# Kernel tuning notes

Hardware: AMD Instinct MI355X
Metric: run time of the kernel (lower is better)

The kernel has to match this reference:

```python
import jax, jax.numpy as jnp
import numpy as np

T, B, H, W_IMG = 8, 4, 128, 128
NUM_CLS = 21
LEAK = 0.99   # config.leak_mem
THR = 1.0     # config.def_threshold
EPS = 1e-4    # BatchNorm2d eps


@jax.custom_vjp
def spike(mem):
    # Heaviside spike with 'Linear' surrogate gradient
    return (mem > THR).astype(mem.dtype)

def _spike_fwd(mem):
    return spike(mem), mem

def _spike_bwd(mem, g):
    # triangular (linear) surrogate around threshold
    return (g * jnp.maximum(0.0, 1.0 - jnp.abs(mem - THR)),)

spike.defvjp(_spike_fwd, _spike_bwd)


def conv(x, w, pad, dil=1):
    return jax.lax.conv_general_dilated(
        x, w, window_strides=(1, 1), padding=[(pad, pad), (pad, pad)],
        rhs_dilation=(dil, dil), dimension_numbers=('NCHW', 'OIHW', 'NCHW'))


def bn_apply(x, bn_t):
    # bn_t: [3, C] = (gamma, running_mean, running_var); bias=None in the model
    g, mu, var = bn_t[0], bn_t[1], bn_t[2]
    inv = (g / jnp.sqrt(var + EPS))[None, :, None, None]
    return (x - mu[None, :, None, None]) * inv


def avgpool(x):
    # AvgPool2d(kernel=3, stride=2, padding=1), count_include_pad=True -> /9
    s = jax.lax.reduce_window(x, 0.0, jax.lax.add, (1, 1, 3, 3), (1, 1, 2, 2),
                              [(0, 0), (0, 0), (1, 1), (1, 1)])
    return s / 9.0


def lif(x, w, bn_t, mem, pad, dil=1):
    # mem = leak*mem + BN_t(conv(x)); spike; soft reset by threshold
    out = bn_apply(conv(x, w, pad, dil), bn_t)
    mem = LEAK * mem + out
    s = spike(mem)
    return mem - THR * s, s


def _forward(x, u, W0, W1, W2, W3, W4, W5, W6, W7, W8,
             bn0, bn1, bn2, bn3, bn4, bn5, bn6, bn7):
    # Poisson generator: spike when u <= |x|, carrying sign of x. [T,B,3,H,W]
    spk_in = jnp.where(u <= jnp.abs(x)[None], jnp.sign(x)[None], 0.0)
    z = lambda c, h: jnp.zeros((B, c, h, h), x.dtype)
    init = (z(64, 128), z(64, 128), z(128, 64), z(128, 64),
            z(256, 32), z(256, 32), z(256, 32), z(1024, 32), z(NUM_CLS, 32))

    def step(carry, xs):
        m0, m1, m2, m3, m4, m5, m6, m7, macc = carry
        sp, b0, b1, b2, b3, b4, b5, b6, b7 = xs
        m0, o = lif(sp, W0, b0, m0, 1)
        m1, o = lif(o, W1, b1, m1, 1)
        o = avgpool(o)                      # 128 -> 64
        m2, o = lif(o, W2, b2, m2, 1)
        m3, o = lif(o, W3, b3, m3, 1)
        o = avgpool(o)                      # 64 -> 32
        m4, o = lif(o, W4, b4, m4, 1)
        m5, o = lif(o, W5, b5, m5, 2, 2)    # atrous256
        m6, o = lif(o, W6, b6, m6, 2, 2)    # atrous256
        m7, o = lif(o, W7, b7, m7, 12, 12)  # classifier atrous1024
        macc = macc + conv(o, W8, 0)        # output layer accumulates voltage
        return (m0, m1, m2, m3, m4, m5, m6, m7, macc), None

    carry, _ = jax.lax.scan(step, init, (spk_in, bn0, bn1, bn2, bn3, bn4, bn5, bn6, bn7))
    return carry[-1] / T


def setup_inputs() -> dict:
    key = jax.random.key(0)
    ks = jax.random.split(key, 24)

    def w(k, shape):
        fan_in = int(np.prod(shape[1:]))
        return jax.random.normal(k, shape, jnp.float32) / np.sqrt(fan_in)

    def bn(k, c):
        return jax.random.uniform(k, (T, 3, c), jnp.float32, 0.25, 1.25)

    inp = {
        'x': jax.random.normal(ks[0], (B, 3, H, W_IMG), jnp.float32),
        'u': jax.random.uniform(ks[1], (T, B, 3, H, W_IMG), jnp.float32),
        'W0': w(ks[2], (64, 3, 3, 3)),
        'W1': w(ks[3], (64, 64, 3, 3)),
        'W2': w(ks[4], (128, 64, 3, 3)),
        'W3': w(ks[5], (128, 128, 3, 3)),
        'W4': w(ks[6], (256, 128, 3, 3)),
        'W5': w(ks[7], (256, 256, 3, 3)),
        'W6': w(ks[8], (256, 256, 3, 3)),
        'W7': w(ks[9], (1024, 256, 3, 3)),
        'W8': w(ks[10], (NUM_CLS, 1024, 1, 1)),
        'bn0': bn(ks[11], 64), 'bn1': bn(ks[12], 64),
        'bn2': bn(ks[13], 128), 'bn3': bn(ks[14], 128),
        'bn4': bn(ks[15], 256), 'bn5': bn(ks[16], 256),
        'bn6': bn(ks[17], 256), 'bn7': bn(ks[18], 1024),
    }
    return inp


def reference(x, u, W0, W1, W2, W3, W4, W5, W6, W7, W8,
              bn0, bn1, bn2, bn3, bn4, bn5, bn6, bn7):
    return _forward(x, u, W0, W1, W2, W3, W4, W5, W6, W7, W8,
                    bn0, bn1, bn2, bn3, bn4, bn5, bn6, bn7)
```

## Files before the change

kernel.cpp:

```cpp
#include <hip/hip_runtime.h>
#include <hip/hip_bf16.h>
#include <cstddef>
#include <cstdint>

#define LEAK  0.99f
#define THRS  1.0f
#define BNEPS 1e-4f

static constexpr int TT   = 8;
static constexpr int BB   = 4;
static constexpr int NCLS = 21;

typedef __attribute__((ext_vector_type(8))) short short8v;
typedef __attribute__((ext_vector_type(4))) float f32x4;

__global__ void zero_f32(float* __restrict__ p, int n) {
  int i = blockIdx.x * blockDim.x + threadIdx.x;
  int stride = gridDim.x * blockDim.x;
  for (; i < n; i += stride) p[i] = 0.0f;
}

__global__ void scale_f32(float* __restrict__ p, int n, float s) {
  int i = blockIdx.x * blockDim.x + threadIdx.x;
  if (i < n) p[i] *= s;
}

__global__ void wsplit(const float* __restrict__ Wsrc,
                       __hip_bfloat16* __restrict__ whi, __hip_bfloat16* __restrict__ wlo,
                       int Co, int Ci, int Cip, float scale) {
  const int Kpad = 9 * Cip;
  const int n = Co * Kpad;
  int i = blockIdx.x * 256 + threadIdx.x;
  if (i >= n) return;
  int co = i / Kpad, k = i - co * Kpad;
  int tap = k / Cip, ci = k - tap * Cip;
  float w = 0.0f;
  if (ci < Ci) w = Wsrc[((size_t)co * Ci + ci) * 9 + tap] * scale;
  __hip_bfloat16 h = __float2bfloat16(w);
  float r = w - __bfloat162float(h);
  whi[i] = h;
  wlo[i] = __float2bfloat16(r);
}

__global__ void spike_gen(const float* __restrict__ x, const float* __restrict__ u,
                          __hip_bfloat16* __restrict__ spk) {
  const int HW = 128 * 128;
  int i = blockIdx.x * 256 + threadIdx.x;
  if (i >= BB * HW) return;
  int b = i / HW, hw = i - b * HW;
#pragma unroll
  for (int c = 0; c < 3; ++c) {
    float xv = x[((size_t)b * 3 + c) * HW + hw];
    float uv = u[((size_t)b * 3 + c) * HW + hw];
    float ax = fabsf(xv);
    float sg = (xv > 0.0f) ? 1.0f : ((xv < 0.0f) ? -1.0f : 0.0f);
    float s  = (uv <= ax) ? sg : 0.0f;
    spk[(size_t)i * 32 + c] = __float2bfloat16(s);
  }
}

template<int M, int N, int GRP, int CPT, int SPLIT>
__global__ __launch_bounds__(SPLIT * 256, 4) void gemm_lif(
    const __hip_bfloat16* __restrict__ actin,
    const __hip_bfloat16* __restrict__ wsp,
    const float* __restrict__ bnt,
    float* __restrict__ mem, __hip_bfloat16* __restrict__ actout,
    const __hip_bfloat16* __restrict__ zp,
    int Co, int lgHW, int lgW, int dil, int lgGX) {
  constexpr int NW = 4;
  constexpr int Cip = CPT * 32;
  constexpr int Kpad = 9 * Cip;
  constexpr int lgcpt = (CPT == 1) ? 0 : (CPT == 2) ? 1 : (CPT == 4) ? 2 : 3;
  constexpr int R  = N * 32;
  constexpr int lgR = (N == 1) ? 5 : ((N == 2) ? 6 : 7);
  constexpr int BUFROWS = GRP * R;
  constexpr int BUFELEM = BUFROWS * 32;
  constexpr int INSTS = BUFROWS / (16 * NW);
  constexpr int AM = M * GRP;
  constexpr int WAITN = AM;
  constexpr int NCH = (9 * CPT) / SPLIT;
  constexpr int NGRP = NCH / GRP;
  static_assert(NCH % GRP == 0, "group must divide per-half chunk count");
  __shared__ __hip_bfloat16 lds[SPLIT * 2 * BUFELEM];

  const int HW = 1 << lgHW, H = HW >> lgW, W = 1 << lgW;
  const unsigned CoKpad = (unsigned)Co * Kpad;
  const int lane = threadIdx.x & 63, wid = threadIdx.x >> 6;
  const int kw = wid >> 2;
  const int wq = wid & 3;
  const int l15 = lane & 15, g = lane >> 4;
  __hip_bfloat16* ldsh = lds + kw * 2 * BUFELEM;

  const int nb = gridDim.x;
  const int flat = blockIdx.x;
  const int swz = (flat & 7) * (nb >> 3) + (flat >> 3);
  const int bx = swz & ((1 << lgGX) - 1);
  const int by = swz >> lgGX;
  const int p0  = (bx * NW + wq) * (M * 16);
  const int co0 = by * (N * 16);

  int b_[M], y_[M], x_[M];
#pragma unroll
  for (int m = 0; m < M; ++m) {
    int pb = p0 + m * 16;
    b_[m] = pb >> lgHW;
    int rem = pb & (HW - 1);
    y_[m] = rem >> lgW;
    x_[m] = (rem & (W - 1)) + l15;
  }

  const unsigned kbase = (unsigned)kw * (NCH * 32);
  unsigned sgb[INSTS];
#pragma unroll
  for (int i = 0; i < INSTS; ++i) {
    int f  = wq * (BUFROWS / NW) + i * 16 + (lane >> 2);
    int cc = f >> lgR;
    int r  = f & (R - 1);
    int half = r >> (lgR - 1);
    int co   = r & (16 * N - 1);
    int slot = (lane & 3) ^ ((co >> 1) & 3);
    sgb[i] = (unsigned)half * CoKpad + (unsigned)(co0 + co) * Kpad + slot * 8
           + cc * 32 + kbase;
  }

  auto stage = [&](int gl, int buf) {
#pragma unroll
    for (int i = 0; i < INSTS; ++i) {
      const __hip_bfloat16* gp = wsp + sgb[i] + gl * (GRP * 32);
      __hip_bfloat16* lp = &ldsh[buf * BUFELEM + (wq * (BUFROWS / NW) + i * 16) * 32];
      __builtin_amdgcn_global_load_lds(
          (const __attribute__((address_space(1))) void*)gp,
          (__attribute__((address_space(3))) void*)lp, 16, 0, 0);
    }
  };

  const __hip_bfloat16* apc[M];
  auto mkaddr = [&](int tap) {
    int ty = (tap * 11) >> 5;
    int tx = tap - ty * 3;
    int dy = (ty - 1) * dil, dx = (tx - 1) * dil;
#pragma unroll
    for (int m = 0; m < M; ++m) {
      int sy = y_[m] + dy, sx = x_[m] + dx;
      bool v = (sy >= 0) & (sy < H) & (sx >= 0) & (sx < W);
      int pix = (b_[m] << lgHW) + (sy << lgW) + sx;
      apc[m] = v ? (actin + (size_t)pix * Cip + 8 * g) : (zp + 8 * g);
    }
  };

  auto prefA = [&](int gl, short8v (&dst)[GRP][M], bool first) {
#pragma unroll
    for (int cc = 0; cc < GRP; ++cc) {
      int c = kw * NCH + gl * GRP + cc;
      if ((c & (CPT - 1)) == 0 || (first && cc == 0)) mkaddr(c >> lgcpt);
      int kc = (c & (CPT - 1)) << 5;
#pragma unroll
      for (int m = 0; m < M; ++m)
        dst[cc][m] = *(const short8v*)(apc[m] + kc);
    }
  };

  f32x4 acc[M][N] = {};
  const int rdb = l15 * 32 + ((g ^ ((l15 >> 1) & 3)) * 8);

  short8v aA[GRP][M], aB[GRP][M];

  auto grp_body = [&](int gi, short8v (&aU)[GRP][M], short8v (&aF)[GRP][M]) {
    asm volatile("s_waitcnt vmcnt(%0)" :: "n"(WAITN) : "memory");
    __builtin_amdgcn_s_barrier();
    __builtin_amdgcn_sched_barrier(0);

    if (gi + 1 < NGRP) {
      stage(gi + 1, (gi + 1) & 1);
      prefA(gi + 1, aF, false);
    }

    const __hip_bfloat16* bp = &ldsh[(gi & 1) * BUFELEM];
#pragma unroll
    for (int cc = 0; cc < GRP; ++cc) {
      short8v bh[N], bl[N];
#pragma unroll
      for (int j = 0; j < N; ++j) {
        bh[j] = *(const short8v*)(bp + cc * (R * 32) + j * 512 + rdb);
        bl[j] = *(const short8v*)(bp + cc * (R * 32) + (N * 512) + j * 512 + rdb);
      }
      __builtin_amdgcn_s_setprio(1);
#pragma unroll
      for (int j = 0; j < N; ++j)
#pragma unroll
        for (int m = 0; m < M; ++m) {
          acc[m][j] = __builtin_amdgcn_mfma_f32_16x16x32_bf16(aU[cc][m], bh[j], acc[m][j], 0, 0, 0);
          acc[m][j] = __builtin_amdgcn_mfma_f32_16x16x32_bf16(aU[cc][m], bl[j], acc[m][j], 0, 0, 0);
        }
      __builtin_amdgcn_s_setprio(0);
    }
  };

  stage(0, 0);
  prefA(0, aA, true);

#pragma unroll
  for (int gi = 0; gi < NGRP; ++gi) {
    if (gi & 1) grp_body(gi, aB, aA);
    else        grp_body(gi, aA, aB);
  }

  if constexpr (SPLIT == 2) {
    asm volatile("s_waitcnt vmcnt(0) lgkmcnt(0)" ::: "memory");
    __builtin_amdgcn_s_barrier();
    f32x4* red = (f32x4*)lds;
    const int rbase = (wq * 64 + lane) * (M * N);
    if (kw == 1) {
#pragma unroll
      for (int m = 0; m < M; ++m)
#pragma unroll
        for (int j = 0; j < N; ++j)
          red[rbase + m * N + j] = acc[m][j];
    }
    asm volatile("s_waitcnt lgkmcnt(0)" ::: "memory");
    __builtin_amdgcn_s_barrier();
    if (kw == 1) return;
#pragma unroll
    for (int m = 0; m < M; ++m)
#pragma unroll
      for (int j = 0; j < N; ++j) {
        f32x4 t = red[rbase + m * N + j];
#pragma unroll
        for (int r = 0; r < 4; ++r) acc[m][j][r] += t[r];
      }
  }

#pragma unroll
  for (int j = 0; j < N; ++j) {
    int c = co0 + j * 16 + l15;
    float ga = bnt[c], mu = bnt[Co + c], va = bnt[2 * Co + c];
    float sc = ga / sqrtf(va + BNEPS);
#pragma unroll
    for (int m = 0; m < M; ++m) {
      int pixb = p0 + m * 16 + 4 * g;
#pragma unroll
      for (int r = 0; r < 4; ++r) {
        size_t idx = (size_t)(pixb + r) * Co + c;
        float bno = (acc[m][j][r] - mu) * sc;
        float mv = LEAK * mem[idx] + bno;
        float s = (mv > THRS) ? 1.0f : 0.0f;
        actout[idx] = __float2bfloat16(s);
        mem[idx] = mv - s;
      }
    }
  }
}

__global__ void avgpool_sum8(const __hip_bfloat16* __restrict__ in,
                             __hip_bfloat16* __restrict__ out, int C, int H, int W) {
  const int Ho = H >> 1, Wo = W >> 1;
  const int C8 = C >> 3;
  const int n = BB * Ho * Wo * C8;
  int i = blockIdx.x * 256 + threadIdx.x;
  if (i >= n) return;
  int c8 = i % C8; int t = i / C8;
  int xo = t % Wo; t /= Wo;
  int yo = t % Ho; int b = t / Ho;
  const int y0 = 2 * yo - 1, x0 = 2 * xo - 1;
  float s[8] = {0, 0, 0, 0, 0, 0, 0, 0};
#pragma unroll
  for (int dy = 0; dy < 3; ++dy) {
    int iy = y0 + dy;
    if (iy < 0 || iy >= H) continue;
#pragma unroll
    for (int dx = 0; dx < 3; ++dx) {
      int ix = x0 + dx;
      if (ix < 0 || ix >= W) continue;
      short8v v = *(const short8v*)(in + (((size_t)b * H + iy) * W + ix) * C + c8 * 8);
#pragma unroll
      for (int e = 0; e < 8; ++e) {
        __hip_bfloat16_raw raw; raw.x = (unsigned short)v[e];
        s[e] += __bfloat162float(__hip_bfloat16(raw));
      }
    }
  }
  short8v o;
#pragma unroll
  for (int e = 0; e < 8; ++e) {
    __hip_bfloat16_raw raw = __hip_bfloat16_raw(__float2bfloat16(s[e]));
    o[e] = (short)raw.x;
  }
  *(short8v*)(out + (size_t)i * 8) = o;
}

__global__ void out_conv(const __hip_bfloat16* __restrict__ act,
                         const float* __restrict__ W8, float* __restrict__ out) {
  int gw = (blockIdx.x * 256 + threadIdx.x) >> 6;
  int lane = threadIdx.x & 63;
  int b = gw >> 10, pix = gw & 1023;
  const __hip_bfloat16* ap = act + ((size_t)gw << 10);
  float acc[NCLS];
#pragma unroll
  for (int c = 0; c < NCLS; ++c) acc[c] = 0.0f;
  for (int j = 0; j < 16; ++j) {
    int ci = j * 64 + lane;
    float av = __bfloat162float(ap[ci]);
#pragma unroll
    for (int c = 0; c < NCLS; ++c) acc[c] = fmaf(av, W8[c * 1024 + ci], acc[c]);
  }
#pragma unroll
  for (int c = 0; c < NCLS; ++c) {
    float v = acc[c];
    for (int off = 32; off; off >>= 1) v += __shfl_xor(v, off, 64);
    if (lane == 0) out[((size_t)b * NCLS + c) * 1024 + pix] += v;
  }
}

extern "C" void kernel_launch(void* const* d_in, const int* in_sizes, int n_in,
                              void* d_out, int out_size, void* d_ws, size_t ws_size,
                              hipStream_t stream) {
  const float* x = (const float*)d_in[0];
  const float* u = (const float*)d_in[1];
  const float* Wc[9];
  for (int i = 0; i < 9; ++i) Wc[i] = (const float*)d_in[2 + i];
  const float* bn[8];
  for (int i = 0; i < 8; ++i) bn[i] = (const float*)d_in[11 + i];

  const int Ci_[8]  = {3, 64, 64, 128, 128, 256, 256, 256};
  const int Cip_[8] = {32, 64, 64, 128, 128, 256, 256, 256};
  const int Co_[8]  = {64, 64, 128, 128, 256, 256, 256, 1024};
  const int HH_[8]  = {128, 128, 64, 64, 32, 32, 32, 32};
  const float wsc_[8] = {1.f, 1.f, 1.f / 9.f, 1.f, 1.f / 9.f, 1.f, 1.f, 1.f};

  float* ws = (float*)d_ws;
  size_t off = 0;
  auto align8 = [](size_t v) { return (v + 7) & ~(size_t)7; };

  float* memp[8];
  for (int i = 0; i < 8; ++i) {
    memp[i] = ws + off;
    off += (size_t)BB * HH_[i] * HH_[i] * Co_[i];
  }
  __hip_bfloat16* spk = (__hip_bfloat16*)(ws + off);
  off += (size_t)BB * 16384 * 32 / 2;
  __hip_bfloat16* zp = (__hip_bfloat16*)(ws + off);
  off += 256;
  const size_t zero_floats = off;
  __hip_bfloat16* actA = (__hip_bfloat16*)(ws + off); off += 2097152;
  __hip_bfloat16* actB = (__hip_bfloat16*)(ws + off); off += 2097152;
  __hip_bfloat16* wall[8];
  for (int i = 0; i < 8; ++i) {
    size_t n = (size_t)Co_[i] * 9 * Cip_[i];
    wall[i] = (__hip_bfloat16*)(ws + off);
    off = align8(off + n);
  }

  zero_f32<<<2048, 256, 0, stream>>>(ws, (int)zero_floats);
  zero_f32<<<(BB * NCLS * 1024 + 255) / 256, 256, 0, stream>>>((float*)d_out, BB * NCLS * 1024);

  for (int i = 0; i < 8; ++i) {
    int n = Co_[i] * 9 * Cip_[i];
    wsplit<<<(n + 255) / 256, 256, 0, stream>>>(Wc[i], wall[i], wall[i] + n,
                                                Co_[i], Ci_[i], Cip_[i], wsc_[i]);
  }

  const size_t uT = (size_t)BB * 3 * 16384;
  for (int t = 0; t < TT; ++t) {
    spike_gen<<<(BB * 16384 + 255) / 256, 256, 0, stream>>>(x, u + (size_t)t * uT, spk);
    gemm_lif<2, 2, 3, 1, 1><<<1024, 256, 0, stream>>>(spk,  wall[0], bn[0] + (size_t)t * 3 * 64,   memp[0], actA, zp, 64,   14, 7, 1, 9);
    gemm_lif<2, 2, 3, 2, 1><<<1024, 256, 0, stream>>>(actA, wall[1], bn[1] + (size_t)t * 3 * 64,   memp[1], actB, zp, 64,   14, 7, 1, 9);
    avgpool_sum8<<<(BB * 64 * 64 * 8 + 255) / 256, 256, 0, stream>>>(actB, actA, 64, 128, 128);
    gemm_lif<2, 2, 3, 2, 2><<<512, 512, 0, stream>>>(actA, wall[2], bn[2] + (size_t)t * 3 * 128,  memp[2], actB, zp, 128,  12, 6, 1, 7);
    gemm_lif<2, 2, 3, 4, 2><<<512, 512, 0, stream>>>(actB, wall[3], bn[3] + (size_t)t * 3 * 128,  memp[3], actA, zp, 128,  12, 6, 1, 7);
    avgpool_sum8<<<(BB * 32 * 32 * 16 + 255) / 256, 256, 0, stream>>>(actA, actB, 128, 64, 64);
    gemm_lif<1, 2, 3, 4, 2><<<512, 512, 0, stream>>>(actB, wall[4], bn[4] + (size_t)t * 3 * 256,   memp[4], actA, zp, 256,  10, 5, 1, 6);
    gemm_lif<1, 2, 4, 8, 2><<<512, 512, 0, stream>>>(actA, wall[5], bn[5] + (size_t)t * 3 * 256,   memp[5], actB, zp, 256,  10, 5, 2, 6);
    gemm_lif<1, 2, 4, 8, 2><<<512, 512, 0, stream>>>(actB, wall[6], bn[6] + (size_t)t * 3 * 256,   memp[6], actA, zp, 256,  10, 5, 2, 6);
    gemm_lif<2, 4, 2, 8, 2><<<512, 512, 0, stream>>>(actA, wall[7], bn[7] + (size_t)t * 3 * 1024, memp[7], actB, zp, 1024, 10, 5, 12, 5);
    out_conv<<<dim3(BB * 1024 / 4), 256, 0, stream>>>(actB, Wc[8], (float*)d_out);
  }
  scale_f32<<<(BB * NCLS * 1024 + 255) / 256, 256, 0, stream>>>((float*)d_out, BB * NCLS * 1024, 1.0f / TT);
}
```

Measured before the change: 2.020 ms.

## Interleave A-operand prefetch with MFMA loop and transpose split-K reduction layout

```diff
diff --git a/kernel.cpp b/kernel.cpp
--- a/kernel.cpp
+++ b/kernel.cpp
@@ -148,16 +148,12 @@
     }
   };
 
-  auto prefA = [&](int gl, short8v (&dst)[GRP][M], bool first) {
-#pragma unroll
-    for (int cc = 0; cc < GRP; ++cc) {
-      int c = kw * NCH + gl * GRP + cc;
-      if ((c & (CPT - 1)) == 0 || (first && cc == 0)) mkaddr(c >> lgcpt);
-      int kc = (c & (CPT - 1)) << 5;
-#pragma unroll
-      for (int m = 0; m < M; ++m)
-        dst[cc][m] = *(const short8v*)(apc[m] + kc);
-    }
+  auto prefA_slice = [&](int cg, int cc, short8v (&dst)[GRP][M], bool force) {
+    if ((cg & (CPT - 1)) == 0 || force) mkaddr(cg >> lgcpt);
+    int kc = (cg & (CPT - 1)) << 5;
+#pragma unroll
+    for (int m = 0; m < M; ++m)
+      dst[cc][m] = *(const short8v*)(apc[m] + kc);
   };
 
   f32x4 acc[M][N] = {};
@@ -170,14 +166,13 @@
     __builtin_amdgcn_s_barrier();
     __builtin_amdgcn_sched_barrier(0);
 
-    if (gi + 1 < NGRP) {
-      stage(gi + 1, (gi + 1) & 1);
-      prefA(gi + 1, aF, false);
-    }
+    const bool more = (gi + 1 < NGRP);
+    if (more) stage(gi + 1, (gi + 1) & 1);
 
     const __hip_bfloat16* bp = &ldsh[(gi & 1) * BUFELEM];
 #pragma unroll
     for (int cc = 0; cc < GRP; ++cc) {
+      if (more) prefA_slice(kw * NCH + (gi + 1) * GRP + cc, cc, aF, false);
       short8v bh[N], bl[N];
 #pragma unroll
       for (int j = 0; j < N; ++j) {
@@ -197,7 +192,9 @@
   };
 
   stage(0, 0);
-  prefA(0, aA, true);
+#pragma unroll
+  for (int cc = 0; cc < GRP; ++cc)
+    prefA_slice(kw * NCH + cc, cc, aA, cc == 0);
 
 #pragma unroll
   for (int gi = 0; gi < NGRP; ++gi) {
@@ -208,14 +205,16 @@
   if constexpr (SPLIT == 2) {
     asm volatile("s_waitcnt vmcnt(0) lgkmcnt(0)" ::: "memory");
     __builtin_amdgcn_s_barrier();
-    f32x4* red = (f32x4*)lds;
-    const int rbase = (wq * 64 + lane) * (M * N);
+    float* red = (float*)lds;
+    const int tid = wq * 64 + lane;
     if (kw == 1) {
 #pragma unroll
       for (int m = 0; m < M; ++m)
 #pragma unroll
         for (int j = 0; j < N; ++j)
-          red[rbase + m * N + j] = acc[m][j];
+#pragma unroll
+          for (int r = 0; r < 4; ++r)
+            red[((m * N + j) * 4 + r) * 256 + tid] = acc[m][j][r];
     }
     asm volatile("s_waitcnt lgkmcnt(0)" ::: "memory");
     __builtin_amdgcn_s_barrier();
@@ -223,11 +222,10 @@
 #pragma unroll
     for (int m = 0; m < M; ++m)
 #pragma unroll
-      for (int j = 0; j < N; ++j) {
-        f32x4 t = red[rbase + m * N + j];
-#pragma unroll
-        for (int r = 0; r < 4; ++r) acc[m][j][r] += t[r];
-      }
+      for (int j = 0; j < N; ++j)
+#pragma unroll
+        for (int r = 0; r < 4; ++r)
+          acc[m][j][r] += red[((m * N + j) * 4 + r) * 256 + tid];
   }
 
 #pragma unroll
```

After: 1.948 ms. -3.6%, faster.
